# Kernel optimization log

Hardware: AMD Instinct MI355X
Metric: run time of the kernel (lower is better)

The kernel has to match this reference:

```python
import jax, jax.numpy as jnp
import numpy as np

C = 2048
N = 8
K = C // N  # 256
B = 4096


def setup_inputs() -> dict:
    key = jax.random.key(0)
    ks = jax.random.split(key, 9)
    s_in = 1.0 / np.sqrt(C)
    s_k = 1.0 / np.sqrt(K)
    return {
        "x": jax.random.normal(ks[0], (B, C), dtype=jnp.float32),
        # weights stored [in, out] (y = x @ W + b), equivalent to torch Linear
        "W_theta": jax.random.uniform(ks[1], (C, K), jnp.float32, -s_in, s_in),
        "b_theta": jax.random.uniform(ks[2], (K,), jnp.float32, -s_in, s_in),
        "W_phi": jax.random.uniform(ks[3], (C, K), jnp.float32, -s_in, s_in),
        "b_phi": jax.random.uniform(ks[4], (K,), jnp.float32, -s_in, s_in),
        "W_f": jax.random.uniform(ks[5], (C, K), jnp.float32, -s_in, s_in),
        "b_f": jax.random.uniform(ks[6], (K,), jnp.float32, -s_in, s_in),
        "W_g": jax.random.uniform(ks[7], (K, C), jnp.float32, -s_k, s_k),
        "b_g": jax.random.uniform(ks[8], (C,), jnp.float32, -s_k, s_k),
    }


def reference(x, W_theta, b_theta, W_phi, b_phi, W_f, b_f, W_g, b_g):
    theta = x @ W_theta + b_theta          # [B, K]
    phi = x @ W_phi + b_phi                # [B, K]
    f = x @ W_f + b_f                      # [B, K]
    # outer product per sample -> [B, K, K], softmax over last dim
    scores = jax.nn.softmax(theta[:, :, None] * phi[:, None, :], axis=-1)
    t = jnp.einsum('bij,bj->bi', scores, f)  # [B, K]
    return x + t @ W_g + b_g               # residual, [B, C]
```

## Files before the change

kernel.cpp:

```cpp
#include <hip/hip_runtime.h>

constexpr int Bsz   = 4096;
constexpr int Cdim  = 2048;
constexpr int Kdim  = 256;
constexpr int PROJW = 3 * Kdim;
constexpr int KSPLIT = 4;

typedef __attribute__((ext_vector_type(8))) short short8;
typedef __attribute__((ext_vector_type(4))) float floatx4;
typedef __attribute__((ext_vector_type(2))) float float2v;
typedef __attribute__((ext_vector_type(4))) _Float16 half4v;

__device__ __forceinline__ unsigned short f2bf(float f) {
    unsigned int u = __float_as_uint(f);
    u += 0x7FFFu + ((u >> 16) & 1u);
    return (unsigned short)(u >> 16);
}

__device__ __forceinline__ void load16(const void* g, void* lds) {
    __builtin_amdgcn_global_load_lds(
        (const __attribute__((address_space(1))) unsigned int*)g,
        (__attribute__((address_space(3))) unsigned int*)lds, 16, 0, 0);
}


__global__ __launch_bounds__(256) void prep_kernel(
    const float* __restrict__ x, unsigned short* __restrict__ xb2,
    const float* __restrict__ Wt, const float* __restrict__ Wp,
    const float* __restrict__ Wf, const float* __restrict__ Wg,
    unsigned short* __restrict__ Wcat2, unsigned short* __restrict__ WgT)
{
    __shared__ float tile[32][33];
    const int bid = blockIdx.x;
    if (bid < 4096) {
        const int i   = bid * 256 + threadIdx.x;
        const int row = i >> 8;
        const int kg  = i & 255;
        const float4* xv = reinterpret_cast<const float4*>(x);
        const float4 v0 = xv[2 * i];
        const float4 v1 = xv[2 * i + 1];
        short8 o;
        o[0] = (short)f2bf(v0.x); o[1] = (short)f2bf(v0.y);
        o[2] = (short)f2bf(v0.z); o[3] = (short)f2bf(v0.w);
        o[4] = (short)f2bf(v1.x); o[5] = (short)f2bf(v1.y);
        o[6] = (short)f2bf(v1.z); o[7] = (short)f2bf(v1.w);
        const size_t dst = ((size_t)(row >> 7) * 64 + (kg >> 2)) * 4096 +
                           (row & 127) * 32 + (kg & 3) * 8;
        *reinterpret_cast<short8*>(xb2 + dst) = o;
        return;
    }
    const int q = bid - 4096;
    const int z = q >> 9;
    const int tileId = q & 511;
    const float* __restrict__ in;
    int R, C;
    if (z < 3) {
        in = (z == 0) ? Wt : (z == 1) ? Wp : Wf;
        R = Cdim; C = Kdim;
    } else {
        in = Wg; R = Kdim; C = Cdim;
    }
    const int ctiles = C / 32;
    const int c0 = (tileId % ctiles) * 32;
    const int r0 = (tileId / ctiles) * 32;
    const int tx = threadIdx.x & 31, ty = threadIdx.x >> 5;
#pragma unroll
    for (int i = ty; i < 32; i += 8)
        tile[i][tx] = in[(size_t)(r0 + i) * C + c0 + tx];
    __syncthreads();
    if (z < 3) {
#pragma unroll
        for (int i = ty; i < 32; i += 8) {
            const int cg = z * 256 + c0 + i;
            Wcat2[((size_t)(cg >> 7) * 64 + (r0 >> 5)) * 4096 +
                  (cg & 127) * 32 + tx] = f2bf(tile[tx][i]);
        }
    } else {
#pragma unroll
        for (int i = ty; i < 32; i += 8)
            WgT[(size_t)(c0 + i) * R + r0 + tx] = f2bf(tile[tx][i]);
    }
}

constexpr int RPS = 152;

__global__ __launch_bounds__(256) void proj_mfma(
    const unsigned short* __restrict__ xb2,
    const unsigned short* __restrict__ Wcat2,
    _Float16* __restrict__ pp)
{
    __shared__ __align__(16) char pool[128 * RPS * 2];
    short* S = (short*)pool;

    const int tid  = threadIdx.x;
    const int lane = tid & 63;
    const int wid  = tid >> 6;
    const int wr   = wid >> 1, wc = wid & 1;

    const int L    = blockIdx.x;
    const int xcd  = L & 7;
    const int slot = L >> 3;
    const int rowTile = xcd * 4 + slot / 6;
    const int colTile = slot % 6;
    const int rowBase = rowTile * 128;
    const int colBase = colTile * 128;
    const int kz      = blockIdx.y;

    floatx4 acc[4][4] = {};

    const unsigned short* gA =
        xb2 + ((size_t)rowTile * 64 + kz * 16) * 4096 + tid * 8;
    const unsigned short* gB =
        Wcat2 + ((size_t)colTile * 64 + kz * 16) * 4096 + tid * 8;

    const int wbase = (tid & ~63) * 8;
    const int mrow = lane & 15;
    const int kgrp = lane >> 4;

    load16(gA, S + wbase);        load16(gA + 2048, S + wbase + 2048);
    load16(gB, S + 8192 + wbase); load16(gB + 2048, S + 8192 + wbase + 2048);
    gA += 4096; gB += 4096;
    asm volatile("s_waitcnt vmcnt(0)" ::: "memory");
    __builtin_amdgcn_s_barrier();
    asm volatile("" ::: "memory");

    int cur = 0;
    for (int kt = 0; kt < 16; ++kt) {
        if (kt < 15) {
            short* An = S + (cur ^ 1) * 4096;
            short* Bn = S + 8192 + (cur ^ 1) * 4096;
            load16(gA, An + wbase);        load16(gA + 2048, An + wbase + 2048);
            load16(gB, Bn + wbase);        load16(gB + 2048, Bn + wbase + 2048);
            gA += 4096; gB += 4096;
        }
        const short* Ac = S + cur * 4096;
        const short* Bc = S + 8192 + cur * 4096;
        short8 af[4], bfr[4];
#pragma unroll
        for (int i = 0; i < 4; ++i)
            af[i]  = *(const short8*)&Ac[(wr * 64 + i * 16 + mrow) * 32 + kgrp * 8];
#pragma unroll
        for (int j = 0; j < 4; ++j)
            bfr[j] = *(const short8*)&Bc[(wc * 64 + j * 16 + mrow) * 32 + kgrp * 8];
#pragma unroll
        for (int i = 0; i < 4; ++i)
#pragma unroll
            for (int j = 0; j < 4; ++j)
                acc[i][j] = __builtin_amdgcn_mfma_f32_16x16x32_bf16(
                    af[i], bfr[j], acc[i][j], 0, 0, 0);
        asm volatile("s_waitcnt vmcnt(0)" ::: "memory");
        __builtin_amdgcn_s_barrier();
        asm volatile("" ::: "memory");
        cur ^= 1;
    }

    _Float16* rp = (_Float16*)pool;
#pragma unroll
    for (int j = 0; j < 4; ++j) {
        const int cL = wc * 64 + j * 16 + mrow;
#pragma unroll
        for (int i = 0; i < 4; ++i)
#pragma unroll
            for (int r = 0; r < 4; ++r)
                rp[(wr * 64 + i * 16 + kgrp * 4 + r) * RPS + cL] =
                    (_Float16)acc[i][j][r];
    }
    __syncthreads();

    _Float16* __restrict__ dst = pp + (size_t)kz * Bsz * PROJW;
#pragma unroll
    for (int it = 0; it < 8; ++it) {
        const int c    = it * 256 + tid;
        const int rowL = c >> 4;
        const int ch   = c & 15;
        const float4 v = *reinterpret_cast<const float4*>(&rp[rowL * RPS + ch * 8]);
        *reinterpret_cast<float4*>(
            &dst[(size_t)(rowBase + rowL) * PROJW + colBase + ch * 8]) = v;
    }
}

__global__ __launch_bounds__(256) void attn_kernel(
    const _Float16* __restrict__ pp,
    const float* __restrict__ bt, const float* __restrict__ bp,
    const float* __restrict__ bff,
    unsigned short* __restrict__ t)
{
    __shared__ float sphi[4][Kdim];
    __shared__ float sff[4][Kdim];

    const int tid = threadIdx.x;
    const int s   = tid >> 6;
    const int l   = tid & 63;
    const int b   = blockIdx.x * 4 + s;
    const int j0  = l * 4;
    const size_t rowOff = (size_t)b * PROJW;

    float4 th = *reinterpret_cast<const float4*>(bt + j0);
    float4 ph = *reinterpret_cast<const float4*>(bp + j0);
    float4 fv = *reinterpret_cast<const float4*>(bff + j0);
#pragma unroll
    for (int z = 0; z < KSPLIT; ++z) {
        const _Float16* __restrict__ r = pp + (size_t)z * Bsz * PROJW + rowOff;
        half4v a = *reinterpret_cast<const half4v*>(r + j0);
        half4v c = *reinterpret_cast<const half4v*>(r + Kdim + j0);
        half4v d = *reinterpret_cast<const half4v*>(r + 2 * Kdim + j0);
        th.x += (float)a.x; th.y += (float)a.y; th.z += (float)a.z; th.w += (float)a.w;
        ph.x += (float)c.x; ph.y += (float)c.y; ph.z += (float)c.z; ph.w += (float)c.w;
        fv.x += (float)d.x; fv.y += (float)d.y; fv.z += (float)d.z; fv.w += (float)d.w;
    }
    const float tl[4] = {th.x * 1.44269504f, th.y * 1.44269504f,
                         th.z * 1.44269504f, th.w * 1.44269504f};
    *reinterpret_cast<float4*>(&sphi[s][j0]) = ph;
    *reinterpret_cast<float4*>(&sff[s][j0])  = fv;
    __syncthreads();

    float2v sa[4][2] = {}, na[4][2] = {};
    const float4* __restrict__ sp  = reinterpret_cast<const float4*>(sphi[s]);
    const float4* __restrict__ sfp = reinterpret_cast<const float4*>(sff[s]);
#pragma unroll 4
    for (int p = 0; p < Kdim / 4; ++p) {
        const float4 ph4 = sp[p];
        const float4 ff4 = sfp[p];
        const float2v p01 = {ph4.x, ph4.y};
        const float2v p23 = {ph4.z, ph4.w};
        const float2v f01 = {ff4.x, ff4.y};
        const float2v f23 = {ff4.z, ff4.w};
#pragma unroll
        for (int i = 0; i < 4; ++i) {
            const float2v a01 = tl[i] * p01;
            const float2v a23 = tl[i] * p23;
            float2v e01, e23;
            e01.x = __builtin_amdgcn_exp2f(a01.x);
            e01.y = __builtin_amdgcn_exp2f(a01.y);
            e23.x = __builtin_amdgcn_exp2f(a23.x);
            e23.y = __builtin_amdgcn_exp2f(a23.y);
            sa[i][0] += e01;
            sa[i][1] += e23;
            na[i][0] += e01 * f01;
            na[i][1] += e23 * f23;
        }
    }
    ushort4 o;
    unsigned short* op = &o.x;
#pragma unroll
    for (int i = 0; i < 4; ++i) {
        const float den = sa[i][0].x + sa[i][0].y + sa[i][1].x + sa[i][1].y;
        const float num = na[i][0].x + na[i][0].y + na[i][1].x + na[i][1].y;
        op[i] = f2bf(num * __builtin_amdgcn_rcpf(den));
    }
    *reinterpret_cast<ushort4*>(t + (size_t)b * Kdim + j0) = o;
}

constexpr int OPS = 68;

__global__ __launch_bounds__(256) void out_mfma(
    const unsigned short* __restrict__ tb,
    const unsigned short* __restrict__ WgT,
    const float* __restrict__ bg,
    const float* __restrict__ x,
    float* __restrict__ out)
{
    __shared__ __align__(16) char pool[128 * OPS * 4];
    short* S = (short*)pool;

    const int tid  = threadIdx.x;
    const int lane = tid & 63;
    const int wid  = tid >> 6;
    const int wr   = wid >> 1, wc = wid & 1;
    const int rowBase = blockIdx.x * 128;
    const int colBase = blockIdx.y * 128;

    floatx4 acc[4][4] = {};

    const unsigned short* gA0 = tb  + (size_t)(rowBase + (tid >> 2)) * Kdim + (tid & 3) * 8;
    const unsigned short* gA1 = tb  + (size_t)(rowBase + 64 + (tid >> 2)) * Kdim + (tid & 3) * 8;
    const unsigned short* gB0 = WgT + (size_t)(colBase + (tid >> 2)) * Kdim + (tid & 3) * 8;
    const unsigned short* gB1 = WgT + (size_t)(colBase + 64 + (tid >> 2)) * Kdim + (tid & 3) * 8;

    const int wbase = (tid & ~63) * 8;
    const int mrow = lane & 15;
    const int kgrp = lane >> 4;

    load16(gA0, S + wbase);        load16(gA1, S + wbase + 2048);
    load16(gB0, S + 8192 + wbase); load16(gB1, S + 8192 + wbase + 2048);
    gA0 += 32; gA1 += 32; gB0 += 32; gB1 += 32;
    asm volatile("s_waitcnt vmcnt(0)" ::: "memory");
    __builtin_amdgcn_s_barrier();
    asm volatile("" ::: "memory");

    int cur = 0;
    for (int kt = 0; kt < 8; ++kt) {
        if (kt < 7) {
            short* An = S + (cur ^ 1) * 4096;
            short* Bn = S + 8192 + (cur ^ 1) * 4096;
            load16(gA0, An + wbase);        load16(gA1, An + wbase + 2048);
            load16(gB0, Bn + wbase);        load16(gB1, Bn + wbase + 2048);
            gA0 += 32; gA1 += 32; gB0 += 32; gB1 += 32;
        }
        const short* Ac = S + cur * 4096;
        const short* Bc = S + 8192 + cur * 4096;
        short8 af[4], bfr[4];
#pragma unroll
        for (int i = 0; i < 4; ++i)
            af[i]  = *(const short8*)&Ac[(wr * 64 + i * 16 + mrow) * 32 + kgrp * 8];
#pragma unroll
        for (int j = 0; j < 4; ++j)
            bfr[j] = *(const short8*)&Bc[(wc * 64 + j * 16 + mrow) * 32 + kgrp * 8];
#pragma unroll
        for (int i = 0; i < 4; ++i)
#pragma unroll
            for (int j = 0; j < 4; ++j)
                acc[i][j] = __builtin_amdgcn_mfma_f32_16x16x32_bf16(
                    af[i], bfr[j], acc[i][j], 0, 0, 0);
        asm volatile("s_waitcnt vmcnt(0)" ::: "memory");
        __builtin_amdgcn_s_barrier();
        asm volatile("" ::: "memory");
        cur ^= 1;
    }

    float* rp = (float*)pool;
#pragma unroll
    for (int h = 0; h < 2; ++h) {
        if (wc == h) {
#pragma unroll
            for (int j = 0; j < 4; ++j) {
                const int cL = j * 16 + mrow;
#pragma unroll
                for (int i = 0; i < 4; ++i)
#pragma unroll
                    for (int r = 0; r < 4; ++r)
                        rp[(wr * 64 + i * 16 + kgrp * 4 + r) * OPS + cL] =
                            acc[i][j][r];
            }
        }
        __syncthreads();
#pragma unroll
        for (int it = 0; it < 8; ++it) {
            const int c    = it * 256 + tid;
            const int rowL = c >> 4;
            const int ch   = c & 15;
            const float4 v = *reinterpret_cast<const float4*>(&rp[rowL * OPS + ch * 4]);
            const int colG = colBase + h * 64 + ch * 4;
            const size_t g = (size_t)(rowBase + rowL) * Cdim + colG;
            const float4 bgv = *reinterpret_cast<const float4*>(bg + colG);
            const float4 xv  = *reinterpret_cast<const float4*>(x + g);
            float4 o;
            o.x = v.x + bgv.x + xv.x;
            o.y = v.y + bgv.y + xv.y;
            o.z = v.z + bgv.z + xv.z;
            o.w = v.w + bgv.w + xv.w;
            *reinterpret_cast<float4*>(out + g) = o;
        }
        __syncthreads();
    }
}

extern "C" void kernel_launch(void* const* d_in, const int* in_sizes, int n_in,
                              void* d_out, int out_size, void* d_ws, size_t ws_size,
                              hipStream_t stream) {
    const float* x  = (const float*)d_in[0];
    const float* Wt = (const float*)d_in[1];
    const float* bt = (const float*)d_in[2];
    const float* Wp = (const float*)d_in[3];
    const float* bp = (const float*)d_in[4];
    const float* Wf = (const float*)d_in[5];
    const float* bf = (const float*)d_in[6];
    const float* Wg = (const float*)d_in[7];
    const float* bg = (const float*)d_in[8];
    float* out = (float*)d_out;

    char* w = (char*)d_ws;
    _Float16*       pp    = (_Float16*)w;
    unsigned short* xb2   = (unsigned short*)(w + 25165824);
    unsigned short* Wcat2 = (unsigned short*)(w + 41943040);
    unsigned short* WgT   = (unsigned short*)(w + 45088768);
    unsigned short* tb    = (unsigned short*)(w + 46137344);

    prep_kernel<<<6144, 256, 0, stream>>>(x, xb2, Wt, Wp, Wf, Wg, Wcat2, WgT);
    proj_mfma<<<dim3(192, KSPLIT), 256, 0, stream>>>(xb2, Wcat2, pp);
    attn_kernel<<<Bsz / 4, 256, 0, stream>>>(pp, bt, bp, bf, tb);
    out_mfma<<<dim3(Bsz / 128, Cdim / 128), 256, 0, stream>>>(tb, WgT, bg, x, out);
}
```

Before: 164.3 us.

## Fuse x fp32-to-bf16 conversion into projection GEMM A-tile loads

```diff
diff --git a/kernel.cpp b/kernel.cpp
--- a/kernel.cpp
+++ b/kernel.cpp
@@ -17,39 +17,25 @@
     return (unsigned short)(u >> 16);
 }
 
+__device__ __forceinline__ unsigned int cvtpk(float a, float b) {
+    unsigned int r;
+    asm("v_cvt_pk_bf16_f32 %0, %1, %2" : "=v"(r) : "v"(a), "v"(b));
+    return r;
+}
+
 __device__ __forceinline__ void load16(const void* g, void* lds) {
     __builtin_amdgcn_global_load_lds(
         (const __attribute__((address_space(1))) unsigned int*)g,
         (__attribute__((address_space(3))) unsigned int*)lds, 16, 0, 0);
 }
 
-
 __global__ __launch_bounds__(256) void prep_kernel(
-    const float* __restrict__ x, unsigned short* __restrict__ xb2,
     const float* __restrict__ Wt, const float* __restrict__ Wp,
     const float* __restrict__ Wf, const float* __restrict__ Wg,
     unsigned short* __restrict__ Wcat2, unsigned short* __restrict__ WgT)
 {
     __shared__ float tile[32][33];
-    const int bid = blockIdx.x;
-    if (bid < 4096) {
-        const int i   = bid * 256 + threadIdx.x;
-        const int row = i >> 8;
-        const int kg  = i & 255;
-        const float4* xv = reinterpret_cast<const float4*>(x);
-        const float4 v0 = xv[2 * i];
-        const float4 v1 = xv[2 * i + 1];
-        short8 o;
-        o[0] = (short)f2bf(v0.x); o[1] = (short)f2bf(v0.y);
-        o[2] = (short)f2bf(v0.z); o[3] = (short)f2bf(v0.w);
-        o[4] = (short)f2bf(v1.x); o[5] = (short)f2bf(v1.y);
-        o[6] = (short)f2bf(v1.z); o[7] = (short)f2bf(v1.w);
-        const size_t dst = ((size_t)(row >> 7) * 64 + (kg >> 2)) * 4096 +
-                           (row & 127) * 32 + (kg & 3) * 8;
-        *reinterpret_cast<short8*>(xb2 + dst) = o;
-        return;
-    }
-    const int q = bid - 4096;
+    const int q = blockIdx.x;
     const int z = q >> 9;
     const int tileId = q & 511;
     const float* __restrict__ in;
@@ -85,7 +71,7 @@
 constexpr int RPS = 152;
 
 __global__ __launch_bounds__(256) void proj_mfma(
-    const unsigned short* __restrict__ xb2,
+    const float* __restrict__ x,
     const unsigned short* __restrict__ Wcat2,
     _Float16* __restrict__ pp)
 {
@@ -108,30 +94,43 @@
 
     floatx4 acc[4][4] = {};
 
-    const unsigned short* gA =
-        xb2 + ((size_t)rowTile * 64 + kz * 16) * 4096 + tid * 8;
+    const float* gx = x + (size_t)(rowBase + (tid >> 1)) * Cdim +
+                      kz * 512 + (tid & 1) * 16;
     const unsigned short* gB =
         Wcat2 + ((size_t)colTile * 64 + kz * 16) * 4096 + tid * 8;
 
     const int wbase = (tid & ~63) * 8;
+    const int aoff  = tid * 16;
     const int mrow = lane & 15;
     const int kgrp = lane >> 4;
 
-    load16(gA, S + wbase);        load16(gA + 2048, S + wbase + 2048);
-    load16(gB, S + 8192 + wbase); load16(gB + 2048, S + 8192 + wbase + 2048);
-    gA += 4096; gB += 4096;
-    asm volatile("s_waitcnt vmcnt(0)" ::: "memory");
-    __builtin_amdgcn_s_barrier();
-    asm volatile("" ::: "memory");
+    {
+        const float4* xv = reinterpret_cast<const float4*>(gx);
+        const float4 v0 = xv[0], v1 = xv[1], v2 = xv[2], v3 = xv[3];
+        load16(gB, S + 8192 + wbase); load16(gB + 2048, S + 8192 + wbase + 2048);
+        gx += 32; gB += 4096;
+        uint4 q0, q1;
+        q0.x = cvtpk(v0.x, v0.y); q0.y = cvtpk(v0.z, v0.w);
+        q0.z = cvtpk(v1.x, v1.y); q0.w = cvtpk(v1.z, v1.w);
+        q1.x = cvtpk(v2.x, v2.y); q1.y = cvtpk(v2.z, v2.w);
+        q1.z = cvtpk(v3.x, v3.y); q1.w = cvtpk(v3.z, v3.w);
+        *reinterpret_cast<uint4*>(S + aoff)     = q0;
+        *reinterpret_cast<uint4*>(S + aoff + 8) = q1;
+        asm volatile("s_waitcnt vmcnt(0)" ::: "memory");
+        asm volatile("s_waitcnt lgkmcnt(0)" ::: "memory");
+        __builtin_amdgcn_s_barrier();
+        asm volatile("" ::: "memory");
+    }
 
     int cur = 0;
     for (int kt = 0; kt < 16; ++kt) {
+        float4 v0, v1, v2, v3;
         if (kt < 15) {
-            short* An = S + (cur ^ 1) * 4096;
+            const float4* xv = reinterpret_cast<const float4*>(gx);
+            v0 = xv[0]; v1 = xv[1]; v2 = xv[2]; v3 = xv[3];
             short* Bn = S + 8192 + (cur ^ 1) * 4096;
-            load16(gA, An + wbase);        load16(gA + 2048, An + wbase + 2048);
-            load16(gB, Bn + wbase);        load16(gB + 2048, Bn + wbase + 2048);
-            gA += 4096; gB += 4096;
+            load16(gB, Bn + wbase); load16(gB + 2048, Bn + wbase + 2048);
+            gx += 32; gB += 4096;
         }
         const short* Ac = S + cur * 4096;
         const short* Bc = S + 8192 + cur * 4096;
@@ -148,7 +147,18 @@
             for (int j = 0; j < 4; ++j)
                 acc[i][j] = __builtin_amdgcn_mfma_f32_16x16x32_bf16(
                     af[i], bfr[j], acc[i][j], 0, 0, 0);
-        asm volatile("s_waitcnt vmcnt(0)" ::: "memory");
+        if (kt < 15) {
+            short* An = S + (cur ^ 1) * 4096;
+            uint4 q0, q1;
+            q0.x = cvtpk(v0.x, v0.y); q0.y = cvtpk(v0.z, v0.w);
+            q0.z = cvtpk(v1.x, v1.y); q0.w = cvtpk(v1.z, v1.w);
+            q1.x = cvtpk(v2.x, v2.y); q1.y = cvtpk(v2.z, v2.w);
+            q1.z = cvtpk(v3.x, v3.y); q1.w = cvtpk(v3.z, v3.w);
+            *reinterpret_cast<uint4*>(An + aoff)     = q0;
+            *reinterpret_cast<uint4*>(An + aoff + 8) = q1;
+            asm volatile("s_waitcnt vmcnt(0)" ::: "memory");
+        }
+        asm volatile("s_waitcnt lgkmcnt(0)" ::: "memory");
         __builtin_amdgcn_s_barrier();
         asm volatile("" ::: "memory");
         cur ^= 1;
@@ -371,13 +381,12 @@
 
     char* w = (char*)d_ws;
     _Float16*       pp    = (_Float16*)w;
-    unsigned short* xb2   = (unsigned short*)(w + 25165824);
-    unsigned short* Wcat2 = (unsigned short*)(w + 41943040);
-    unsigned short* WgT   = (unsigned short*)(w + 45088768);
-    unsigned short* tb    = (unsigned short*)(w + 46137344);
-
-    prep_kernel<<<6144, 256, 0, stream>>>(x, xb2, Wt, Wp, Wf, Wg, Wcat2, WgT);
-    proj_mfma<<<dim3(192, KSPLIT), 256, 0, stream>>>(xb2, Wcat2, pp);
+    unsigned short* Wcat2 = (unsigned short*)(w + 25165824);
+    unsigned short* WgT   = (unsigned short*)(w + 28311552);
+    unsigned short* tb    = (unsigned short*)(w + 29360128);
+
+    prep_kernel<<<2048, 256, 0, stream>>>(Wt, Wp, Wf, Wg, Wcat2, WgT);
+    proj_mfma<<<dim3(192, KSPLIT), 256, 0, stream>>>(x, Wcat2, pp);
     attn_kernel<<<Bsz / 4, 256, 0, stream>>>(pp, bt, bp, bf, tb);
     out_mfma<<<dim3(Bsz / 128, Cdim / 128), 256, 0, stream>>>(tb, WgT, bg, x, out);
 }
```

Result: slower. 172.8 us (+5.2%).

## Widen projection GEMM tiles to 128x192 and fold K-split into XCD-aware grid

Applied to the files above, without the earlier changes.

```diff
diff --git a/kernel.cpp b/kernel.cpp
--- a/kernel.cpp
+++ b/kernel.cpp
@@ -22,7 +22,6 @@
         (const __attribute__((address_space(1))) unsigned int*)g,
         (__attribute__((address_space(3))) unsigned int*)lds, 16, 0, 0);
 }
-
 
 __global__ __launch_bounds__(256) void prep_kernel(
     const float* __restrict__ x, unsigned short* __restrict__ xb2,
@@ -72,8 +71,10 @@
 #pragma unroll
         for (int i = ty; i < 32; i += 8) {
             const int cg = z * 256 + c0 + i;
-            Wcat2[((size_t)(cg >> 7) * 64 + (r0 >> 5)) * 4096 +
-                  (cg & 127) * 32 + tx] = f2bf(tile[tx][i]);
+            const int ct = cg / 192;
+            const int cr = cg - ct * 192;
+            Wcat2[((size_t)ct * 64 + (r0 >> 5)) * 6144 + cr * 32 + tx] =
+                f2bf(tile[tx][i]);
         }
     } else {
 #pragma unroll
@@ -82,7 +83,7 @@
     }
 }
 
-constexpr int RPS = 152;
+constexpr int RPS = 200;
 
 __global__ __launch_bounds__(256) void proj_mfma(
     const unsigned short* __restrict__ xb2,
@@ -100,26 +101,30 @@
     const int L    = blockIdx.x;
     const int xcd  = L & 7;
     const int slot = L >> 3;
-    const int rowTile = xcd * 4 + slot / 6;
-    const int colTile = slot % 6;
+    const int rowTile = xcd * 4 + (slot >> 4);
+    const int colTile = (slot >> 2) & 3;
+    const int kz      = slot & 3;
     const int rowBase = rowTile * 128;
-    const int colBase = colTile * 128;
-    const int kz      = blockIdx.y;
-
-    floatx4 acc[4][4] = {};
+    const int colBase = colTile * 192;
+
+    floatx4 acc[4][6] = {};
 
     const unsigned short* gA =
-        xb2 + ((size_t)rowTile * 64 + kz * 16) * 4096 + tid * 8;
+        xb2 + ((size_t)rowTile * 64 + kz * 16) * 4096 + wid * 1024 + lane * 8;
     const unsigned short* gB =
-        Wcat2 + ((size_t)colTile * 64 + kz * 16) * 4096 + tid * 8;
-
-    const int wbase = (tid & ~63) * 8;
+        Wcat2 + ((size_t)colTile * 64 + kz * 16) * 6144 + wid * 1536 + lane * 8;
+
+    const int aoff = wid * 1024;
+    const int boff = wid * 1536;
     const int mrow = lane & 15;
     const int kgrp = lane >> 4;
 
-    load16(gA, S + wbase);        load16(gA + 2048, S + wbase + 2048);
-    load16(gB, S + 8192 + wbase); load16(gB + 2048, S + 8192 + wbase + 2048);
-    gA += 4096; gB += 4096;
+    load16(gA,        S + aoff);
+    load16(gA + 512,  S + aoff + 512);
+    load16(gB,        S + 8192 + boff);
+    load16(gB + 512,  S + 8192 + boff + 512);
+    load16(gB + 1024, S + 8192 + boff + 1024);
+    gA += 4096; gB += 6144;
     asm volatile("s_waitcnt vmcnt(0)" ::: "memory");
     __builtin_amdgcn_s_barrier();
     asm volatile("" ::: "memory");
@@ -128,24 +133,27 @@
     for (int kt = 0; kt < 16; ++kt) {
         if (kt < 15) {
             short* An = S + (cur ^ 1) * 4096;
-            short* Bn = S + 8192 + (cur ^ 1) * 4096;
-            load16(gA, An + wbase);        load16(gA + 2048, An + wbase + 2048);
-            load16(gB, Bn + wbase);        load16(gB + 2048, Bn + wbase + 2048);
-            gA += 4096; gB += 4096;
+            short* Bn = S + 8192 + (cur ^ 1) * 6144;
+            load16(gA,        An + aoff);
+            load16(gA + 512,  An + aoff + 512);
+            load16(gB,        Bn + boff);
+            load16(gB + 512,  Bn + boff + 512);
+            load16(gB + 1024, Bn + boff + 1024);
+            gA += 4096; gB += 6144;
         }
         const short* Ac = S + cur * 4096;
-        const short* Bc = S + 8192 + cur * 4096;
-        short8 af[4], bfr[4];
+        const short* Bc = S + 8192 + cur * 6144;
+        short8 af[4], bfr[6];
 #pragma unroll
         for (int i = 0; i < 4; ++i)
             af[i]  = *(const short8*)&Ac[(wr * 64 + i * 16 + mrow) * 32 + kgrp * 8];
 #pragma unroll
-        for (int j = 0; j < 4; ++j)
-            bfr[j] = *(const short8*)&Bc[(wc * 64 + j * 16 + mrow) * 32 + kgrp * 8];
-#pragma unroll
-        for (int i = 0; i < 4; ++i)
-#pragma unroll
-            for (int j = 0; j < 4; ++j)
+        for (int j = 0; j < 6; ++j)
+            bfr[j] = *(const short8*)&Bc[(wc * 96 + j * 16 + mrow) * 32 + kgrp * 8];
+#pragma unroll
+        for (int i = 0; i < 4; ++i)
+#pragma unroll
+            for (int j = 0; j < 6; ++j)
                 acc[i][j] = __builtin_amdgcn_mfma_f32_16x16x32_bf16(
                     af[i], bfr[j], acc[i][j], 0, 0, 0);
         asm volatile("s_waitcnt vmcnt(0)" ::: "memory");
@@ -156,8 +164,8 @@
 
     _Float16* rp = (_Float16*)pool;
 #pragma unroll
-    for (int j = 0; j < 4; ++j) {
-        const int cL = wc * 64 + j * 16 + mrow;
+    for (int j = 0; j < 6; ++j) {
+        const int cL = wc * 96 + j * 16 + mrow;
 #pragma unroll
         for (int i = 0; i < 4; ++i)
 #pragma unroll
@@ -169,10 +177,10 @@
 
     _Float16* __restrict__ dst = pp + (size_t)kz * Bsz * PROJW;
 #pragma unroll
-    for (int it = 0; it < 8; ++it) {
+    for (int it = 0; it < 12; ++it) {
         const int c    = it * 256 + tid;
-        const int rowL = c >> 4;
-        const int ch   = c & 15;
+        const int rowL = c / 24;
+        const int ch   = c % 24;
         const float4 v = *reinterpret_cast<const float4*>(&rp[rowL * RPS + ch * 8]);
         *reinterpret_cast<float4*>(
             &dst[(size_t)(rowBase + rowL) * PROJW + colBase + ch * 8]) = v;
@@ -377,7 +385,7 @@
     unsigned short* tb    = (unsigned short*)(w + 46137344);
 
     prep_kernel<<<6144, 256, 0, stream>>>(x, xb2, Wt, Wp, Wf, Wg, Wcat2, WgT);
-    proj_mfma<<<dim3(192, KSPLIT), 256, 0, stream>>>(xb2, Wcat2, pp);
+    proj_mfma<<<512, 256, 0, stream>>>(xb2, Wcat2, pp);
     attn_kernel<<<Bsz / 4, 256, 0, stream>>>(pp, bt, bp, bf, tb);
     out_mfma<<<dim3(Bsz / 128, Cdim / 128), 256, 0, stream>>>(tb, WgT, bg, x, out);
 }
```

New measurement: 166.0 us. About the same (+1.0%).
